# Kernel tuning notes

Hardware: AMD Instinct MI355X
Metric: run time of the kernel (lower is better)

Reference implementation:

```python
import jax, jax.numpy as jnp
import numpy as np

B, N, C, H = 16, 4096, 256, 4
D = C // H


def setup_inputs() -> dict:
    key = jax.random.key(0)
    ks = jax.random.split(key, 16)
    s = 0.02
    inp = {
        "x": jax.random.normal(ks[0], (B, N, C), jnp.float32),
        "encoding": jax.random.normal(ks[1], (2, B, 1, N, D), jnp.float32),
        "Wqkv_w": jax.random.normal(ks[2], (3 * C, C), jnp.float32) * s,
        "Wqkv_b": jnp.zeros((3 * C,), jnp.float32),
        "tssa_qkv_w": jax.random.normal(ks[3], (C, C), jnp.float32) * s,
        "tssa_qkv_b": jnp.zeros((C,), jnp.float32),
        "temp": jnp.ones((H, 1), jnp.float32),
        "tssa_out_w": jax.random.normal(ks[4], (C, C), jnp.float32) * s,
        "tssa_out_b": jnp.zeros((C,), jnp.float32),
        "out_proj_w": jax.random.normal(ks[5], (C, C), jnp.float32) * s,
        "out_proj_b": jnp.zeros((C,), jnp.float32),
        "ffn1_w": jax.random.normal(ks[6], (2 * C, 2 * C), jnp.float32) * s,
        "ffn1_b": jnp.zeros((2 * C,), jnp.float32),
        "ln_g": jnp.ones((2 * C,), jnp.float32),
        "ln_b": jnp.zeros((2 * C,), jnp.float32),
        "ffn2_w": jax.random.normal(ks[7], (C, 2 * C), jnp.float32) * s,
        "ffn2_b": jnp.zeros((C,), jnp.float32),
    }
    return inp


def _rotate_half(t):
    # (..., d) -> pairwise rotate: (x1, x2) -> (-x2, x1)
    t2 = t.reshape(t.shape[:-1] + (-1, 2))
    x1, x2 = t2[..., 0], t2[..., 1]
    return jnp.stack((-x2, x1), axis=-1).reshape(t.shape)


def reference(x, encoding, Wqkv_w, Wqkv_b, tssa_qkv_w, tssa_qkv_b, temp,
              tssa_out_w, tssa_out_b, out_proj_w, out_proj_b,
              ffn1_w, ffn1_b, ln_g, ln_b, ffn2_w, ffn2_b):
    b, n, c = x.shape
    h, d = H, D
    # QKV projection, layout (h, d, 3) on last dim as in unflatten(-1,(h,-1,3))
    qkv = (x @ Wqkv_w.T + Wqkv_b).reshape(b, n, h, d, 3).transpose(0, 2, 1, 3, 4)  # b h n d 3
    q, k, v = qkv[..., 0], qkv[..., 1], qkv[..., 2]
    rope = lambda t: t * encoding[0] + _rotate_half(t) * encoding[1]
    q = rope(q)
    k = rope(k)
    flat = lambda t: t.transpose(0, 2, 1, 3).reshape(b, n, c)  # b h n d -> b n (h d)
    w_input = (flat(q) + flat(k) + flat(v)) / 3.0
    # TSSA attention
    w = (w_input @ tssa_qkv_w.T + tssa_qkv_b).reshape(b, n, h, d).transpose(0, 2, 1, 3)  # b h n d
    norm = jnp.sqrt(jnp.sum(w * w, axis=2, keepdims=True))  # L2 over sequence axis N
    w_normed = w / jnp.maximum(norm, 1e-12)
    sum_ws = jnp.sum(w_normed * w_normed, axis=-1)  # b h n
    Pi = jax.nn.softmax(sum_ws * temp[None, :, :], axis=1)  # softmax over heads
    Pi_norm = Pi / (jnp.sum(Pi, axis=-1, keepdims=True) + 1e-8)
    dots = jnp.einsum('bhn,bhnd->bh', Pi_norm, w * w)  # (b,h,1,d) summed over d
    attn = 1.0 / (1.0 + dots)  # b h
    out = -(w * Pi[..., None]) * attn[:, :, None, None]  # b h n d
    out = out.transpose(0, 2, 1, 3).reshape(b, n, c)
    context = out @ tssa_out_w.T + tssa_out_b
    message = context @ out_proj_w.T + out_proj_b
    # residual FFN
    cat = jnp.concatenate([x, message], axis=-1)  # b n 2c
    h1 = cat @ ffn1_w.T + ffn1_b
    mu = jnp.mean(h1, axis=-1, keepdims=True)
    var = jnp.mean((h1 - mu) ** 2, axis=-1, keepdims=True)
    ln = (h1 - mu) / jnp.sqrt(var + 1e-5) * ln_g + ln_b
    g = jax.nn.gelu(ln, approximate=False)
    return x + (g @ ffn2_w.T + ffn2_b)
```

## Files before the change

kernel.cpp:

```cpp
#include <hip/hip_runtime.h>
#include <math.h>

#define Bc 16
#define Nc 4096

typedef __attribute__((ext_vector_type(8))) short short8;
typedef __attribute__((ext_vector_type(4))) float floatx4;

__device__ __forceinline__ unsigned short f2bf(float f) {
    union { float f; unsigned int u; } v; v.f = f;
    unsigned int u = v.u;
    return (unsigned short)((u + 0x7fffu + ((u >> 16) & 1u)) >> 16);
}
__device__ __forceinline__ float bf2f(unsigned short u) {
    union { unsigned int u; float f; } v; v.u = ((unsigned int)u) << 16;
    return v.f;
}

__device__ __forceinline__ void gll16(const unsigned short* g, unsigned short* l) {
    __builtin_amdgcn_global_load_lds(
        (const __attribute__((address_space(1))) void*)g,
        (__attribute__((address_space(3))) void*)l,
        16, 0, 0);
}

template <int EPI, typename TOUT>
__global__ __launch_bounds__(256) void gemm_bf(
    const unsigned short* __restrict__ A0, int lda0,
    const unsigned short* __restrict__ A1, int lda1, int K0,
    const unsigned short* __restrict__ W,
    const float* __restrict__ bias,
    const unsigned short* __restrict__ resid_bf,
    const float* __restrict__ Pi,
    const float* __restrict__ attnb,
    const float* __restrict__ lnstats,
    const float* __restrict__ ln_g,
    const float* __restrict__ ln_b,
    float* __restrict__ norm2,
    float* __restrict__ rowstats,
    TOUT* __restrict__ C, int N, int K)
{
    __shared__ alignas(16) unsigned short As[128 * 64];
    __shared__ alignas(16) unsigned short Bs[128 * 64];

    const int t = threadIdx.x;
    const int bn = blockIdx.x, bm = blockIdx.y;
    const int lane = t & 63, wave = t >> 6;
    const int wm = wave >> 1, wn = wave & 1;
    const int quad = lane >> 4, l16 = lane & 15;
    const int rt = t >> 3, st = t & 7;

    floatx4 acc[4][4];
    #pragma unroll
    for (int i = 0; i < 4; ++i)
        #pragma unroll
        for (int j = 0; j < 4; ++j)
            acc[i][j] = (floatx4){0.f, 0.f, 0.f, 0.f};

    for (int k0 = 0; k0 < K; k0 += 64) {
        #pragma unroll
        for (int hh = 0; hh < 4; ++hh) {
            const int row = hh * 32 + rt;
            const int kseg = st ^ (row & 7);
            const int col = k0 + kseg * 8;
            unsigned short* ldsa = As + row * 64 + st * 8;
            const size_t grow = (size_t)bm * 128 + row;
            if constexpr (EPI == 2) {
                const int b = (int)(grow >> 12);
                const int hd = col >> 6;
                const float sc = -Pi[grow * 4 + hd] * attnb[b * 4 + hd];
                const short8 a = *(const short8*)(A0 + grow * (size_t)lda0 + col);
                short8 o;
                #pragma unroll
                for (int j = 0; j < 8; ++j) o[j] = (short)f2bf(bf2f((unsigned short)a[j]) * sc);
                *(short8*)ldsa = o;
            } else if constexpr (EPI == 3) {
                const float2 stv = *(const float2*)(lnstats + grow * 2);
                const float mean = stv.x * (1.f / 512.f);
                const float var = stv.y * (1.f / 512.f) - mean * mean;
                const float rstd = rsqrtf(var + 1e-5f);
                const short8 a = *(const short8*)(A0 + grow * (size_t)lda0 + col);
                const float4 g0 = *(const float4*)(ln_g + col);
                const float4 g1 = *(const float4*)(ln_g + col + 4);
                const float4 b0 = *(const float4*)(ln_b + col);
                const float4 b1 = *(const float4*)(ln_b + col + 4);
                const float vg[8] = {g0.x, g0.y, g0.z, g0.w, g1.x, g1.y, g1.z, g1.w};
                const float vb[8] = {b0.x, b0.y, b0.z, b0.w, b1.x, b1.y, b1.z, b1.w};
                short8 o;
                #pragma unroll
                for (int j = 0; j < 8; ++j) {
                    const float ln = (bf2f((unsigned short)a[j]) - mean) * rstd * vg[j] + vb[j];
                    o[j] = (short)f2bf(0.5f * ln * (1.f + erff(ln * 0.70710678118654752f)));
                }
                *(short8*)ldsa = o;
            } else {
                const unsigned short* src = (col < K0)
                    ? (A0 + grow * (size_t)lda0 + col)
                    : (A1 + grow * (size_t)lda1 + (col - K0));
                gll16(src, ldsa);
            }
            gll16(W + ((size_t)bn * 128 + row) * (size_t)K + col, Bs + row * 64 + st * 8);
        }
        __syncthreads();
        #pragma unroll
        for (int kk = 0; kk < 2; ++kk) {
            short8 af[4], wf[4];
            #pragma unroll
            for (int i = 0; i < 4; ++i) {
                const int ra = wm * 64 + i * 16 + l16;
                af[i] = *(const short8*)(As + ra * 64 + ((quad + kk * 4) ^ (ra & 7)) * 8);
                const int rw = wn * 64 + i * 16 + l16;
                wf[i] = *(const short8*)(Bs + rw * 64 + ((quad + kk * 4) ^ (rw & 7)) * 8);
            }
            #pragma unroll
            for (int mi = 0; mi < 4; ++mi)
                #pragma unroll
                for (int ni = 0; ni < 4; ++ni)
                    acc[mi][ni] = __builtin_amdgcn_mfma_f32_16x16x32_bf16(
                        wf[ni], af[mi], acc[mi][ni], 0, 0, 0);
        }
        __syncthreads();
    }

    float cs[4][4];
    float rs[4], rq[4];
    if constexpr (EPI == 1) {
        #pragma unroll
        for (int n = 0; n < 4; ++n)
            #pragma unroll
            for (int r = 0; r < 4; ++r) cs[n][r] = 0.f;
    }
    if constexpr (EPI == 4) {
        #pragma unroll
        for (int m = 0; m < 4; ++m) { rs[m] = 0.f; rq[m] = 0.f; }
    }

    #pragma unroll
    for (int mi = 0; mi < 4; ++mi) {
        const size_t row = (size_t)bm * 128 + wm * 64 + mi * 16 + l16;
        #pragma unroll
        for (int ni = 0; ni < 4; ++ni) {
            const int cb = bn * 128 + wn * 64 + ni * 16 + quad * 4;
            const float4 b4 = *(const float4*)(bias + cb);
            float v[4] = {acc[mi][ni][0] + b4.x, acc[mi][ni][1] + b4.y,
                          acc[mi][ni][2] + b4.z, acc[mi][ni][3] + b4.w};
            if constexpr (EPI == 3) {
                const ushort4 xr = *(const ushort4*)(resid_bf + row * (size_t)N + cb);
                v[0] += bf2f(xr.x); v[1] += bf2f(xr.y);
                v[2] += bf2f(xr.z); v[3] += bf2f(xr.w);
            }
            if constexpr (EPI == 1) {
                #pragma unroll
                for (int rg = 0; rg < 4; ++rg) cs[ni][rg] += v[rg] * v[rg];
            }
            if constexpr (EPI == 4) {
                #pragma unroll
                for (int rg = 0; rg < 4; ++rg) { rs[mi] += v[rg]; rq[mi] += v[rg] * v[rg]; }
            }
            if constexpr (__is_same(TOUT, float)) {
                float4 o; o.x = v[0]; o.y = v[1]; o.z = v[2]; o.w = v[3];
                *(float4*)(C + row * (size_t)N + cb) = o;
            } else {
                ushort4 o;
                o.x = f2bf(v[0]); o.y = f2bf(v[1]); o.z = f2bf(v[2]); o.w = f2bf(v[3]);
                *(ushort4*)(C + row * (size_t)N + cb) = o;
            }
        }
    }
    if constexpr (EPI == 1) {
        #pragma unroll
        for (int ni = 0; ni < 4; ++ni)
            #pragma unroll
            for (int rg = 0; rg < 4; ++rg) {
                float s = cs[ni][rg];
                s += __shfl_xor(s, 1, 64);
                s += __shfl_xor(s, 2, 64);
                s += __shfl_xor(s, 4, 64);
                s += __shfl_xor(s, 8, 64);
                if (l16 == 0)
                    atomicAdd(&norm2[(bm >> 5) * 256 + bn * 128 + wn * 64 + ni * 16 + quad * 4 + rg], s);
            }
    }
    if constexpr (EPI == 4) {
        #pragma unroll
        for (int mi = 0; mi < 4; ++mi) {
            float s = rs[mi], q = rq[mi];
            s += __shfl_xor(s, 16, 64); s += __shfl_xor(s, 32, 64);
            q += __shfl_xor(q, 16, 64); q += __shfl_xor(q, 32, 64);
            if (quad == 0) {
                const size_t row = (size_t)bm * 128 + wm * 64 + mi * 16 + l16;
                atomicAdd(&rowstats[row * 2], s);
                atomicAdd(&rowstats[row * 2 + 1], q);
            }
        }
    }
}

__global__ __launch_bounds__(256) void gemm_rope(
    const unsigned short* __restrict__ A,
    const unsigned short* __restrict__ Wsv,
    const float* __restrict__ bsv,
    const float* __restrict__ enc,
    unsigned short* __restrict__ wi)
{
    __shared__ alignas(16) unsigned short As[128 * 32];
    __shared__ alignas(16) unsigned short Ss[128 * 32];
    __shared__ alignas(16) unsigned short Vs[128 * 32];

    const int t = threadIdx.x;
    const int bn = blockIdx.x;
    const int bm = blockIdx.y;
    const int lane = t & 63, wave = t >> 6;
    const int wm = wave >> 1, wn = wave & 1;
    const int quad = lane >> 4, l16 = lane & 15;
    const int rA = t >> 2, cA = (t & 3) * 8;

    floatx4 accs[4][4], accv[4][4];
    #pragma unroll
    for (int i = 0; i < 4; ++i)
        #pragma unroll
        for (int j = 0; j < 4; ++j) {
            accs[i][j] = (floatx4){0.f, 0.f, 0.f, 0.f};
            accv[i][j] = (floatx4){0.f, 0.f, 0.f, 0.f};
        }

    for (int k0 = 0; k0 < 256; k0 += 32) {
        #pragma unroll
        for (int hh = 0; hh < 2; ++hh) {
            const int r = rA + hh * 64;
            gll16(A + ((size_t)bm * 128 + r) * 256 + k0 + cA, &As[t * 8 + hh * 2048]);
            gll16(Wsv + (size_t)(bn * 128 + r) * 256 + k0 + cA, &Ss[t * 8 + hh * 2048]);
            gll16(Wsv + (size_t)(256 + bn * 128 + r) * 256 + k0 + cA, &Vs[t * 8 + hh * 2048]);
        }
        __syncthreads();

        short8 af[4], sf[4], vf[4];
        #pragma unroll
        for (int i = 0; i < 4; ++i) {
            af[i] = *(const short8*)(&As[(wm * 64 + i * 16 + l16) * 32 + quad * 8]);
            sf[i] = *(const short8*)(&Ss[(wn * 64 + i * 16 + l16) * 32 + quad * 8]);
            vf[i] = *(const short8*)(&Vs[(wn * 64 + i * 16 + l16) * 32 + quad * 8]);
        }
        #pragma unroll
        for (int mi = 0; mi < 4; ++mi)
            #pragma unroll
            for (int ni = 0; ni < 4; ++ni) {
                accs[mi][ni] = __builtin_amdgcn_mfma_f32_16x16x32_bf16(af[mi], sf[ni], accs[mi][ni], 0, 0, 0);
                accv[mi][ni] = __builtin_amdgcn_mfma_f32_16x16x32_bf16(af[mi], vf[ni], accv[mi][ni], 0, 0, 0);
            }
        __syncthreads();
    }

    #pragma unroll
    for (int ni = 0; ni < 4; ++ni) {
        const int cg = bn * 128 + wn * 64 + ni * 16 + l16;
        const int d = cg & 63;
        const float sign = (d & 1) ? 1.f : -1.f;
        const float bs = bsv[cg], bv = bsv[256 + cg];
        #pragma unroll
        for (int mi = 0; mi < 4; ++mi) {
            const int rowb = bm * 128 + wm * 64 + mi * 16 + quad * 4;
            #pragma unroll
            for (int rg = 0; rg < 4; ++rg) {
                const size_t row = (size_t)rowb + rg;
                const float sv = accs[mi][ni][rg] + bs;
                const float vv = accv[mi][ni][rg] + bv;
                const float partner = __shfl_xor(sv, 1, 64);
                const size_t eo = row * 64 + d;
                const float e0 = enc[eo];
                const float e1 = enc[4194304 + eo];
                const float r = sv * e0 + sign * partner * e1;
                wi[row * 256 + cg] = f2bf((r + vv) * (1.f / 3.f));
            }
        }
    }
}

__device__ __forceinline__ void conv8(const float* src, unsigned short* dst, int i) {
    const float4 f0 = *(const float4*)(src + (size_t)i * 8);
    const float4 f1 = *(const float4*)(src + (size_t)i * 8 + 4);
    short8 sv;
    sv[0] = (short)f2bf(f0.x); sv[1] = (short)f2bf(f0.y);
    sv[2] = (short)f2bf(f0.z); sv[3] = (short)f2bf(f0.w);
    sv[4] = (short)f2bf(f1.x); sv[5] = (short)f2bf(f1.y);
    sv[6] = (short)f2bf(f1.z); sv[7] = (short)f2bf(f1.w);
    *(short8*)(dst + (size_t)i * 8) = sv;
}

__global__ __launch_bounds__(256) void prep_all(
    const float* __restrict__ x, const float* __restrict__ Wqkv,
    const float* __restrict__ bqkv, const float* __restrict__ tssa_w,
    const float* __restrict__ op_w, const float* __restrict__ to_w,
    const float* __restrict__ to_b, const float* __restrict__ op_b,
    const float* __restrict__ f1w, const float* __restrict__ f2w,
    unsigned short* __restrict__ x_bf, unsigned short* __restrict__ Wsv,
    float* __restrict__ bsv, unsigned short* __restrict__ tssa_bf,
    unsigned short* __restrict__ Wf, float* __restrict__ bfb,
    unsigned short* __restrict__ ffn1_bf, unsigned short* __restrict__ ffn2_bf,
    float* __restrict__ zbase, float* __restrict__ rowstats)
{
    const int blk = blockIdx.x, tt = threadIdx.x;
    if (blk < 8192) {
        conv8(x, x_bf, blk * 256 + tt);
    } else if (blk < 8704) {
        const int r = blk - 8192, c = tt;
        const int cd = r & 255;
        const int h = cd >> 6, dd = cd & 63;
        const int base = h * 192 + dd * 3;
        if (r < 256) {
            Wsv[r * 256 + c] = f2bf(Wqkv[(base + 0) * 256 + c] + Wqkv[(base + 1) * 256 + c]);
            if (c == 0) bsv[r] = bqkv[base] + bqkv[base + 1];
        } else {
            Wsv[r * 256 + c] = f2bf(Wqkv[(base + 2) * 256 + c]);
            if (c == 0) bsv[r] = bqkv[base + 2];
        }
    } else if (blk < 8960) {
        const int i = blk - 8704;
        float s = 0.f;
        for (int k = 0; k < 256; ++k) s += op_w[i * 256 + k] * to_w[k * 256 + tt];
        Wf[i * 256 + tt] = f2bf(s);
    } else if (blk == 8960) {
        float s = op_b[tt];
        for (int k = 0; k < 256; ++k) s += op_w[tt * 256 + k] * to_b[k];
        bfb[tt] = s;
    } else if (blk < 8993) {
        conv8(tssa_w, tssa_bf, (blk - 8961) * 256 + tt);
    } else if (blk < 9121) {
        conv8(f1w, ffn1_bf, (blk - 8993) * 256 + tt);
    } else if (blk < 9185) {
        conv8(f2w, ffn2_bf, (blk - 9121) * 256 + tt);
    } else {
        const int i = (blk - 9185) * 256 + tt;
        if (i < 4288) zbase[i] = 0.f;
        else if (i < 135360) rowstats[i - 4288] = 0.f;
    }
}

__global__ __launch_bounds__(256) void pi_kernel(const unsigned short* __restrict__ w,
                                                 const float* __restrict__ norm2,
                                                 const float* __restrict__ temp,
                                                 float* __restrict__ Pi,
                                                 float* __restrict__ S,
                                                 float* __restrict__ T) {
    const int t = threadIdx.x;
    const int i = t & 15;
    const int lr = t >> 4;
    const size_t r = (size_t)blockIdx.x * 16 + lr;
    const int b = (int)(r >> 12);
    const unsigned short* wrow = w + r * 256;
    const float* n2row = norm2 + b * 256;
    float raw[4], nrm[4];
    #pragma unroll
    for (int h = 0; h < 4; ++h) {
        const ushort4 wv = *(const ushort4*)(wrow + h * 64 + i * 4);
        const float w0 = bf2f(wv.x), w1 = bf2f(wv.y), w2 = bf2f(wv.z), w3 = bf2f(wv.w);
        const float4 n2 = *(const float4*)(n2row + h * 64 + i * 4);
        const float s0 = w0 * w0, s1 = w1 * w1, s2 = w2 * w2, s3 = w3 * w3;
        raw[h] = s0 + s1 + s2 + s3;
        nrm[h] = s0 / fmaxf(n2.x, 1e-24f) + s1 / fmaxf(n2.y, 1e-24f)
               + s2 / fmaxf(n2.z, 1e-24f) + s3 / fmaxf(n2.w, 1e-24f);
    }
    #pragma unroll
    for (int off = 1; off < 16; off <<= 1) {
        #pragma unroll
        for (int h = 0; h < 4; ++h) {
            raw[h] += __shfl_xor(raw[h], off, 64);
            nrm[h] += __shfl_xor(nrm[h], off, 64);
        }
    }
    float sw[4], m = -1e30f;
    #pragma unroll
    for (int h = 0; h < 4; ++h) { sw[h] = nrm[h] * temp[h]; m = fmaxf(m, sw[h]); }
    float e[4], Z = 0.f;
    #pragma unroll
    for (int h = 0; h < 4; ++h) { e[h] = expf(sw[h] - m); Z += e[h]; }
    const float invZ = 1.f / Z;
    float pi[4];
    #pragma unroll
    for (int h = 0; h < 4; ++h) pi[h] = e[h] * invZ;
    if (i < 4) Pi[r * 4 + i] = pi[i];

    __shared__ float sS[16][4], sT[16][4];
    if (i == 0) {
        #pragma unroll
        for (int h = 0; h < 4; ++h) { sS[lr][h] = pi[h]; sT[lr][h] = pi[h] * raw[h]; }
    }
    __syncthreads();
    if (t < 4) {
        float as = 0.f, at = 0.f;
        for (int rr = 0; rr < 16; ++rr) { as += sS[rr][t]; at += sT[rr][t]; }
        atomicAdd(&S[b * 4 + t], as);
        atomicAdd(&T[b * 4 + t], at);
    }
}

__global__ void attn_kernel(const float* __restrict__ S, const float* __restrict__ T,
                            float* __restrict__ attn) {
    const int i = threadIdx.x;
    const float dots = T[i] / (S[i] + 1e-8f);
    attn[i] = 1.f / (1.f + dots);
}

extern "C" void kernel_launch(void* const* d_in, const int* in_sizes, int n_in,
                              void* d_out, int out_size, void* d_ws, size_t ws_size,
                              hipStream_t stream) {
    (void)in_sizes; (void)n_in; (void)out_size; (void)ws_size;
    const float* x          = (const float*)d_in[0];
    const float* enc        = (const float*)d_in[1];
    const float* Wqkv_w     = (const float*)d_in[2];
    const float* Wqkv_b     = (const float*)d_in[3];
    const float* tssa_qkv_w = (const float*)d_in[4];
    const float* tssa_qkv_b = (const float*)d_in[5];
    const float* temp       = (const float*)d_in[6];
    const float* tssa_out_w = (const float*)d_in[7];
    const float* tssa_out_b = (const float*)d_in[8];
    const float* out_proj_w = (const float*)d_in[9];
    const float* out_proj_b = (const float*)d_in[10];
    const float* ffn1_w     = (const float*)d_in[11];
    const float* ffn1_b     = (const float*)d_in[12];
    const float* ln_g       = (const float*)d_in[13];
    const float* ln_b       = (const float*)d_in[14];
    const float* ffn2_w     = (const float*)d_in[15];
    const float* ffn2_b     = (const float*)d_in[16];
    float* outp = (float*)d_out;

    const int M = Bc * Nc;

    char* ws = (char*)d_ws;
    unsigned short* x_bf  = (unsigned short*)(ws);
    unsigned short* wi_bf = (unsigned short*)(ws + (size_t)(32 << 20));
    unsigned short* h1_bf = (unsigned short*)(ws + (size_t)(32 << 20));
    unsigned short* w_bf  = (unsigned short*)(ws + (size_t)(64 << 20));
    unsigned short* msg_bf= (unsigned short*)(ws + (size_t)(96 << 20));
    float* fb    = (float*)(ws + (size_t)(128 << 20));
    float* Pi    = fb;
    float* norm2 = Pi + 262144;
    float* Sb    = norm2 + 4096;
    float* Tb    = Sb + 64;
    float* attnb = Tb + 64;
    float* bsv   = attnb + 64;
    float* bfb   = bsv + 512;
    float* rowstats = bfb + 256;
    unsigned short* Wsv_bf  = (unsigned short*)(rowstats + 131072);
    unsigned short* tssa_bf = Wsv_bf + 131072;
    unsigned short* Wf_bf   = tssa_bf + 65536;
    unsigned short* ffn1_bf = Wf_bf + 65536;
    unsigned short* ffn2_bf = ffn1_bf + 262144;

    prep_all<<<9714, 256, 0, stream>>>(
        x, Wqkv_w, Wqkv_b, tssa_qkv_w, out_proj_w, tssa_out_w, tssa_out_b,
        out_proj_b, ffn1_w, ffn2_w,
        x_bf, Wsv_bf, bsv, tssa_bf, Wf_bf, bfb, ffn1_bf, ffn2_bf,
        norm2, rowstats);

    gemm_rope<<<dim3(2, M / 128), 256, 0, stream>>>(x_bf, Wsv_bf, bsv, enc, wi_bf);

    gemm_bf<1, unsigned short><<<dim3(2, M / 128), 256, 0, stream>>>(
        wi_bf, 256, wi_bf, 256, 256, tssa_bf, tssa_qkv_b,
        nullptr, nullptr, nullptr, nullptr, nullptr, nullptr,
        norm2, nullptr, w_bf, 256, 256);

    pi_kernel<<<4096, 256, 0, stream>>>(w_bf, norm2, temp, Pi, Sb, Tb);
    attn_kernel<<<1, 64, 0, stream>>>(Sb, Tb, attnb);

    gemm_bf<2, unsigned short><<<dim3(2, M / 128), 256, 0, stream>>>(
        w_bf, 256, w_bf, 256, 256, Wf_bf, bfb,
        nullptr, Pi, attnb, nullptr, nullptr, nullptr,
        nullptr, nullptr, msg_bf, 256, 256);

    gemm_bf<4, unsigned short><<<dim3(4, M / 128), 256, 0, stream>>>(
        x_bf, 256, msg_bf, 256, 256, ffn1_bf, ffn1_b,
        nullptr, nullptr, nullptr, nullptr, nullptr, nullptr,
        nullptr, rowstats, h1_bf, 512, 512);

    gemm_bf<3, float><<<dim3(2, M / 128), 256, 0, stream>>>(
        h1_bf, 512, h1_bf, 512, 512, ffn2_bf, ffn2_b,
        x_bf, nullptr, nullptr, rowstats, ln_g, ln_b,
        nullptr, nullptr, outp, 256, 512);
}
```

Before: 512.0 us.

## Widen GEMM tiles to 128x256 with 512 threads and split LN-GELU into standalone kernel

```diff
diff --git a/kernel.cpp b/kernel.cpp
--- a/kernel.cpp
+++ b/kernel.cpp
@@ -25,7 +25,7 @@
 }
 
 template <int EPI, typename TOUT>
-__global__ __launch_bounds__(256) void gemm_bf(
+__global__ __launch_bounds__(512) void gemm_bf(
     const unsigned short* __restrict__ A0, int lda0,
     const unsigned short* __restrict__ A1, int lda1, int K0,
     const unsigned short* __restrict__ W,
@@ -33,20 +33,17 @@
     const unsigned short* __restrict__ resid_bf,
     const float* __restrict__ Pi,
     const float* __restrict__ attnb,
-    const float* __restrict__ lnstats,
-    const float* __restrict__ ln_g,
-    const float* __restrict__ ln_b,
     float* __restrict__ norm2,
     float* __restrict__ rowstats,
     TOUT* __restrict__ C, int N, int K)
 {
     __shared__ alignas(16) unsigned short As[128 * 64];
-    __shared__ alignas(16) unsigned short Bs[128 * 64];
+    __shared__ alignas(16) unsigned short Bs[256 * 64];
 
     const int t = threadIdx.x;
     const int bn = blockIdx.x, bm = blockIdx.y;
     const int lane = t & 63, wave = t >> 6;
-    const int wm = wave >> 1, wn = wave & 1;
+    const int wm = wave >> 2, wn = wave & 3;
     const int quad = lane >> 4, l16 = lane & 15;
     const int rt = t >> 3, st = t & 7;
 
@@ -59,10 +56,9 @@
 
     for (int k0 = 0; k0 < K; k0 += 64) {
         #pragma unroll
-        for (int hh = 0; hh < 4; ++hh) {
-            const int row = hh * 32 + rt;
-            const int kseg = st ^ (row & 7);
-            const int col = k0 + kseg * 8;
+        for (int hh = 0; hh < 2; ++hh) {
+            const int row = hh * 64 + rt;
+            const int col = k0 + (st ^ (row & 7)) * 8;
             unsigned short* ldsa = As + row * 64 + st * 8;
             const size_t grow = (size_t)bm * 128 + row;
             if constexpr (EPI == 2) {
@@ -74,32 +70,18 @@
                 #pragma unroll
                 for (int j = 0; j < 8; ++j) o[j] = (short)f2bf(bf2f((unsigned short)a[j]) * sc);
                 *(short8*)ldsa = o;
-            } else if constexpr (EPI == 3) {
-                const float2 stv = *(const float2*)(lnstats + grow * 2);
-                const float mean = stv.x * (1.f / 512.f);
-                const float var = stv.y * (1.f / 512.f) - mean * mean;
-                const float rstd = rsqrtf(var + 1e-5f);
-                const short8 a = *(const short8*)(A0 + grow * (size_t)lda0 + col);
-                const float4 g0 = *(const float4*)(ln_g + col);
-                const float4 g1 = *(const float4*)(ln_g + col + 4);
-                const float4 b0 = *(const float4*)(ln_b + col);
-                const float4 b1 = *(const float4*)(ln_b + col + 4);
-                const float vg[8] = {g0.x, g0.y, g0.z, g0.w, g1.x, g1.y, g1.z, g1.w};
-                const float vb[8] = {b0.x, b0.y, b0.z, b0.w, b1.x, b1.y, b1.z, b1.w};
-                short8 o;
-                #pragma unroll
-                for (int j = 0; j < 8; ++j) {
-                    const float ln = (bf2f((unsigned short)a[j]) - mean) * rstd * vg[j] + vb[j];
-                    o[j] = (short)f2bf(0.5f * ln * (1.f + erff(ln * 0.70710678118654752f)));
-                }
-                *(short8*)ldsa = o;
             } else {
                 const unsigned short* src = (col < K0)
                     ? (A0 + grow * (size_t)lda0 + col)
                     : (A1 + grow * (size_t)lda1 + (col - K0));
                 gll16(src, ldsa);
             }
-            gll16(W + ((size_t)bn * 128 + row) * (size_t)K + col, Bs + row * 64 + st * 8);
+        }
+        #pragma unroll
+        for (int hh = 0; hh < 4; ++hh) {
+            const int row = hh * 64 + rt;
+            const int col = k0 + (st ^ (row & 7)) * 8;
+            gll16(W + ((size_t)bn * 256 + row) * (size_t)K + col, Bs + row * 64 + st * 8);
         }
         __syncthreads();
         #pragma unroll
@@ -122,14 +104,7 @@
         __syncthreads();
     }
 
-    float cs[4][4];
     float rs[4], rq[4];
-    if constexpr (EPI == 1) {
-        #pragma unroll
-        for (int n = 0; n < 4; ++n)
-            #pragma unroll
-            for (int r = 0; r < 4; ++r) cs[n][r] = 0.f;
-    }
     if constexpr (EPI == 4) {
         #pragma unroll
         for (int m = 0; m < 4; ++m) { rs[m] = 0.f; rq[m] = 0.f; }
@@ -140,7 +115,7 @@
         const size_t row = (size_t)bm * 128 + wm * 64 + mi * 16 + l16;
         #pragma unroll
         for (int ni = 0; ni < 4; ++ni) {
-            const int cb = bn * 128 + wn * 64 + ni * 16 + quad * 4;
+            const int cb = bn * 256 + wn * 64 + ni * 16 + quad * 4;
             const float4 b4 = *(const float4*)(bias + cb);
             float v[4] = {acc[mi][ni][0] + b4.x, acc[mi][ni][1] + b4.y,
                           acc[mi][ni][2] + b4.z, acc[mi][ni][3] + b4.w};
@@ -149,13 +124,23 @@
                 v[0] += bf2f(xr.x); v[1] += bf2f(xr.y);
                 v[2] += bf2f(xr.z); v[3] += bf2f(xr.w);
             }
+            if constexpr (EPI == 4) {
+                #pragma unroll
+                for (int rg = 0; rg < 4; ++rg) { rs[mi] += v[rg]; rq[mi] += v[rg] * v[rg]; }
+            }
             if constexpr (EPI == 1) {
-                #pragma unroll
-                for (int rg = 0; rg < 4; ++rg) cs[ni][rg] += v[rg] * v[rg];
-            }
-            if constexpr (EPI == 4) {
-                #pragma unroll
-                for (int rg = 0; rg < 4; ++rg) { rs[mi] += v[rg]; rq[mi] += v[rg] * v[rg]; }
+                float cs[4];
+                #pragma unroll
+                for (int rg = 0; rg < 4; ++rg) cs[rg] = v[rg] * v[rg];
+                #pragma unroll
+                for (int rg = 0; rg < 4; ++rg) {
+                    float s = cs[rg];
+                    s += __shfl_xor(s, 1, 64);
+                    s += __shfl_xor(s, 2, 64);
+                    s += __shfl_xor(s, 4, 64);
+                    s += __shfl_xor(s, 8, 64);
+                    if (l16 == 0) atomicAdd(&norm2[(bm >> 5) * 256 + cb + rg], s);
+                }
             }
             if constexpr (__is_same(TOUT, float)) {
                 float4 o; o.x = v[0]; o.y = v[1]; o.z = v[2]; o.w = v[3];
@@ -166,20 +151,6 @@
                 *(ushort4*)(C + row * (size_t)N + cb) = o;
             }
         }
-    }
-    if constexpr (EPI == 1) {
-        #pragma unroll
-        for (int ni = 0; ni < 4; ++ni)
-            #pragma unroll
-            for (int rg = 0; rg < 4; ++rg) {
-                float s = cs[ni][rg];
-                s += __shfl_xor(s, 1, 64);
-                s += __shfl_xor(s, 2, 64);
-                s += __shfl_xor(s, 4, 64);
-                s += __shfl_xor(s, 8, 64);
-                if (l16 == 0)
-                    atomicAdd(&norm2[(bm >> 5) * 256 + bn * 128 + wn * 64 + ni * 16 + quad * 4 + rg], s);
-            }
     }
     if constexpr (EPI == 4) {
         #pragma unroll
@@ -203,17 +174,16 @@
     const float* __restrict__ enc,
     unsigned short* __restrict__ wi)
 {
-    __shared__ alignas(16) unsigned short As[128 * 32];
-    __shared__ alignas(16) unsigned short Ss[128 * 32];
-    __shared__ alignas(16) unsigned short Vs[128 * 32];
+    __shared__ alignas(16) unsigned short As[128 * 64];
+    __shared__ alignas(16) unsigned short Ss[128 * 64];
+    __shared__ alignas(16) unsigned short Vs[128 * 64];
 
     const int t = threadIdx.x;
-    const int bn = blockIdx.x;
-    const int bm = blockIdx.y;
+    const int bn = blockIdx.x, bm = blockIdx.y;
     const int lane = t & 63, wave = t >> 6;
     const int wm = wave >> 1, wn = wave & 1;
     const int quad = lane >> 4, l16 = lane & 15;
-    const int rA = t >> 2, cA = (t & 3) * 8;
+    const int rt = t >> 3, st = t & 7;
 
     floatx4 accs[4][4], accv[4][4];
     #pragma unroll
@@ -224,56 +194,95 @@
             accv[i][j] = (floatx4){0.f, 0.f, 0.f, 0.f};
         }
 
-    for (int k0 = 0; k0 < 256; k0 += 32) {
-        #pragma unroll
-        for (int hh = 0; hh < 2; ++hh) {
-            const int r = rA + hh * 64;
-            gll16(A + ((size_t)bm * 128 + r) * 256 + k0 + cA, &As[t * 8 + hh * 2048]);
-            gll16(Wsv + (size_t)(bn * 128 + r) * 256 + k0 + cA, &Ss[t * 8 + hh * 2048]);
-            gll16(Wsv + (size_t)(256 + bn * 128 + r) * 256 + k0 + cA, &Vs[t * 8 + hh * 2048]);
+    for (int k0 = 0; k0 < 256; k0 += 64) {
+        #pragma unroll
+        for (int hh = 0; hh < 4; ++hh) {
+            const int row = hh * 32 + rt;
+            const int col = k0 + (st ^ (row & 7)) * 8;
+            gll16(A + ((size_t)bm * 128 + row) * 256 + col, As + row * 64 + st * 8);
+            gll16(Wsv + (size_t)(bn * 128 + row) * 256 + col, Ss + row * 64 + st * 8);
+            gll16(Wsv + (size_t)(256 + bn * 128 + row) * 256 + col, Vs + row * 64 + st * 8);
         }
         __syncthreads();
-
-        short8 af[4], sf[4], vf[4];
-        #pragma unroll
-        for (int i = 0; i < 4; ++i) {
-            af[i] = *(const short8*)(&As[(wm * 64 + i * 16 + l16) * 32 + quad * 8]);
-            sf[i] = *(const short8*)(&Ss[(wn * 64 + i * 16 + l16) * 32 + quad * 8]);
-            vf[i] = *(const short8*)(&Vs[(wn * 64 + i * 16 + l16) * 32 + quad * 8]);
-        }
-        #pragma unroll
-        for (int mi = 0; mi < 4; ++mi)
+        #pragma unroll
+        for (int kk = 0; kk < 2; ++kk) {
+            short8 af[4], sf[4], vf[4];
             #pragma unroll
-            for (int ni = 0; ni < 4; ++ni) {
-                accs[mi][ni] = __builtin_amdgcn_mfma_f32_16x16x32_bf16(af[mi], sf[ni], accs[mi][ni], 0, 0, 0);
-                accv[mi][ni] = __builtin_amdgcn_mfma_f32_16x16x32_bf16(af[mi], vf[ni], accv[mi][ni], 0, 0, 0);
-            }
+            for (int i = 0; i < 4; ++i) {
+                const int ra = wm * 64 + i * 16 + l16;
+                af[i] = *(const short8*)(As + ra * 64 + ((quad + kk * 4) ^ (ra & 7)) * 8);
+                const int rw = wn * 64 + i * 16 + l16;
+                sf[i] = *(const short8*)(Ss + rw * 64 + ((quad + kk * 4) ^ (rw & 7)) * 8);
+                vf[i] = *(const short8*)(Vs + rw * 64 + ((quad + kk * 4) ^ (rw & 7)) * 8);
+            }
+            #pragma unroll
+            for (int mi = 0; mi < 4; ++mi)
+                #pragma unroll
+                for (int ni = 0; ni < 4; ++ni) {
+                    accs[mi][ni] = __builtin_amdgcn_mfma_f32_16x16x32_bf16(sf[ni], af[mi], accs[mi][ni], 0, 0, 0);
+                    accv[mi][ni] = __builtin_amdgcn_mfma_f32_16x16x32_bf16(vf[ni], af[mi], accv[mi][ni], 0, 0, 0);
+                }
+        }
         __syncthreads();
     }
 
     #pragma unroll
-    for (int ni = 0; ni < 4; ++ni) {
-        const int cg = bn * 128 + wn * 64 + ni * 16 + l16;
-        const int d = cg & 63;
-        const float sign = (d & 1) ? 1.f : -1.f;
-        const float bs = bsv[cg], bv = bsv[256 + cg];
-        #pragma unroll
-        for (int mi = 0; mi < 4; ++mi) {
-            const int rowb = bm * 128 + wm * 64 + mi * 16 + quad * 4;
-            #pragma unroll
-            for (int rg = 0; rg < 4; ++rg) {
-                const size_t row = (size_t)rowb + rg;
-                const float sv = accs[mi][ni][rg] + bs;
-                const float vv = accv[mi][ni][rg] + bv;
-                const float partner = __shfl_xor(sv, 1, 64);
-                const size_t eo = row * 64 + d;
-                const float e0 = enc[eo];
-                const float e1 = enc[4194304 + eo];
-                const float r = sv * e0 + sign * partner * e1;
-                wi[row * 256 + cg] = f2bf((r + vv) * (1.f / 3.f));
-            }
-        }
-    }
+    for (int mi = 0; mi < 4; ++mi) {
+        const size_t row = (size_t)bm * 128 + wm * 64 + mi * 16 + l16;
+        #pragma unroll
+        for (int ni = 0; ni < 4; ++ni) {
+            const int cb = bn * 128 + wn * 64 + ni * 16 + quad * 4;
+            const int d = cb & 63;
+            const float s0 = accs[mi][ni][0] + bsv[cb];
+            const float s1 = accs[mi][ni][1] + bsv[cb + 1];
+            const float s2 = accs[mi][ni][2] + bsv[cb + 2];
+            const float s3 = accs[mi][ni][3] + bsv[cb + 3];
+            const float v0 = accv[mi][ni][0] + bsv[256 + cb];
+            const float v1 = accv[mi][ni][1] + bsv[256 + cb + 1];
+            const float v2 = accv[mi][ni][2] + bsv[256 + cb + 2];
+            const float v3 = accv[mi][ni][3] + bsv[256 + cb + 3];
+            const float4 e0q = *(const float4*)(enc + row * 64 + d);
+            const float4 e1q = *(const float4*)(enc + 4194304 + row * 64 + d);
+            const float r0 = s0 * e0q.x - s1 * e1q.x;
+            const float r1 = s1 * e0q.y + s0 * e1q.y;
+            const float r2 = s2 * e0q.z - s3 * e1q.z;
+            const float r3 = s3 * e0q.w + s2 * e1q.w;
+            ushort4 o;
+            o.x = f2bf((r0 + v0) * (1.f / 3.f));
+            o.y = f2bf((r1 + v1) * (1.f / 3.f));
+            o.z = f2bf((r2 + v2) * (1.f / 3.f));
+            o.w = f2bf((r3 + v3) * (1.f / 3.f));
+            *(ushort4*)(wi + row * 256 + cb) = o;
+        }
+    }
+}
+
+__global__ __launch_bounds__(256) void lngelu_kernel(unsigned short* __restrict__ h1,
+                                                     const float* __restrict__ rowstats,
+                                                     const float* __restrict__ g,
+                                                     const float* __restrict__ bb) {
+    const size_t gid = (size_t)blockIdx.x * 256 + threadIdx.x;
+    const size_t row = gid >> 6;
+    const int col = (int)(gid & 63) * 8;
+    const float2 stv = *(const float2*)(rowstats + row * 2);
+    const float mean = stv.x * (1.f / 512.f);
+    const float var = stv.y * (1.f / 512.f) - mean * mean;
+    const float rstd = rsqrtf(var + 1e-5f);
+    unsigned short* p = h1 + row * 512 + col;
+    const short8 hv = *(const short8*)p;
+    const float4 g0 = *(const float4*)(g + col);
+    const float4 g1 = *(const float4*)(g + col + 4);
+    const float4 b0 = *(const float4*)(bb + col);
+    const float4 b1 = *(const float4*)(bb + col + 4);
+    const float vg[8] = {g0.x, g0.y, g0.z, g0.w, g1.x, g1.y, g1.z, g1.w};
+    const float vb[8] = {b0.x, b0.y, b0.z, b0.w, b1.x, b1.y, b1.z, b1.w};
+    short8 ov;
+    #pragma unroll
+    for (int k = 0; k < 8; ++k) {
+        const float ln = (bf2f((unsigned short)hv[k]) - mean) * rstd * vg[k] + vb[k];
+        ov[k] = (short)f2bf(0.5f * ln * (1.f + erff(ln * 0.70710678118654752f)));
+    }
+    *(short8*)p = ov;
 }
 
 __device__ __forceinline__ void conv8(const float* src, unsigned short* dst, int i) {
@@ -455,26 +464,24 @@
 
     gemm_rope<<<dim3(2, M / 128), 256, 0, stream>>>(x_bf, Wsv_bf, bsv, enc, wi_bf);
 
-    gemm_bf<1, unsigned short><<<dim3(2, M / 128), 256, 0, stream>>>(
+    gemm_bf<1, unsigned short><<<dim3(1, M / 128), 512, 0, stream>>>(
         wi_bf, 256, wi_bf, 256, 256, tssa_bf, tssa_qkv_b,
-        nullptr, nullptr, nullptr, nullptr, nullptr, nullptr,
-        norm2, nullptr, w_bf, 256, 256);
+        nullptr, nullptr, nullptr, norm2, nullptr, w_bf, 256, 256);
 
     pi_kernel<<<4096, 256, 0, stream>>>(w_bf, norm2, temp, Pi, Sb, Tb);
     attn_kernel<<<1, 64, 0, stream>>>(Sb, Tb, attnb);
 
-    gemm_bf<2, unsigned short><<<dim3(2, M / 128), 256, 0, stream>>>(
+    gemm_bf<2, unsigned short><<<dim3(1, M / 128), 512, 0, stream>>>(
         w_bf, 256, w_bf, 256, 256, Wf_bf, bfb,
-        nullptr, Pi, attnb, nullptr, nullptr, nullptr,
-        nullptr, nullptr, msg_bf, 256, 256);
-
-    gemm_bf<4, unsigned short><<<dim3(4, M / 128), 256, 0, stream>>>(
+        nullptr, Pi, attnb, nullptr, nullptr, msg_bf, 256, 256);
+
+    gemm_bf<4, unsigned short><<<dim3(2, M / 128), 512, 0, stream>>>(
         x_bf, 256, msg_bf, 256, 256, ffn1_bf, ffn1_b,
-        nullptr, nullptr, nullptr, nullptr, nullptr, nullptr,
-        nullptr, rowstats, h1_bf, 512, 512);
-
-    gemm_bf<3, float><<<dim3(2, M / 128), 256, 0, stream>>>(
+        nullptr, nullptr, nullptr, nullptr, rowstats, h1_bf, 512, 512);
+
+    lngelu_kernel<<<16384, 256, 0, stream>>>(h1_bf, rowstats, ln_g, ln_b);
+
+    gemm_bf<3, float><<<dim3(1, M / 128), 512, 0, stream>>>(
         h1_bf, 512, h1_bf, 512, 512, ffn2_bf, ffn2_b,
-        x_bf, nullptr, nullptr, rowstats, ln_g, ln_b,
-        nullptr, nullptr, outp, 256, 512);
-}
+        x_bf, nullptr, nullptr, nullptr, nullptr, outp, 256, 512);
+}
```

Result: faster. 456.7 us (-10.8%).
